# Kernel optimization log

Measured on AMD Instinct MI355X. Metric: run time of the kernel, lower is better.

Reference implementation:

```python
import jax, jax.numpy as jnp
import numpy as np

B, LQ, LK, C = 16, 1024, 1024, 512
WH = int(LQ ** 0.5)  # 32


def setup_inputs() -> dict:
    key = jax.random.key(0)
    ks = jax.random.split(key, 6)
    s1 = 1.0 / np.sqrt(LK)
    return {
        "query": jax.random.normal(ks[0], (B, LQ, C), jnp.float32),
        "key": jax.random.normal(ks[1], (B, LK, C), jnp.float32),
        "value": jax.random.normal(ks[2], (B, LK, C), jnp.float32),
        # nn.Linear weights, stored [out_features, in_features] like torch
        "w1": jax.random.normal(ks[3], (LK, LK), jnp.float32) * s1,
        "w2": jax.random.normal(ks[4], (LK, LK), jnp.float32) * s1,
        "w3": jax.random.normal(ks[5], (1, LK), jnp.float32) * s1,
    }


def reference(query, key, value, w1, w2, w3):
    # cosine-similarity matrix (computed under no_grad in the original)
    q = query / 100.0
    k = key / 100.0
    qn = jnp.sqrt(jnp.sum(q * q, axis=-1))[:, :, None]   # [B, LQ, 1]
    kn = jnp.sqrt(jnp.sum(k * k, axis=-1))[:, None, :]   # [B, 1, LK]
    outer = qn * kn                                       # rank-1 outer product [B, LQ, LK]
    upper = jnp.einsum('bqc,bkc->bqk', q, k)              # [B, LQ, LK]
    similar_rev = jax.lax.stop_gradient(upper / (outer + 1e-6))

    # 3-layer MLP gating over the LK axis -> scalar weight per query row
    h = jax.nn.gelu(jnp.einsum('bqk,ok->bqo', similar_rev, w1), approximate=False)
    h = jax.nn.gelu(jnp.einsum('bqk,ok->bqo', h, w2), approximate=False)
    w = jnp.einsum('bqk,ok->bqo', h, w3)[..., 0]          # [B, LQ]

    # weight^T @ similar_rev / wh, then tanh -> per-key scalar gate [B, LK, 1]
    weight = jnp.einsum('bq,bqk->bk', w, similar_rev) / WH
    weight = jnp.tanh(weight)[:, :, None]

    # value modulation + residual
    return value * weight + value
```

## Files before the change

### kernel.cpp

```cpp
#include <hip/hip_runtime.h>
#include <hip/hip_bf16.h>

#define B_  16
#define LQ_ 1024
#define LK_ 1024
#define C_  512

typedef __attribute__((ext_vector_type(4))) float f32x4;
typedef __attribute__((ext_vector_type(8))) short bf16x8;

__device__ __forceinline__ float bf2f(ushort u) {
  union { unsigned int i; float f; } v; v.i = ((unsigned int)u) << 16; return v.f;
}
__device__ __forceinline__ ushort f2bf(float f) {
  union { float f; unsigned int i; } v; v.f = f;
  unsigned int r = v.i + 0x7fffu + ((v.i >> 16) & 1u);
  return (ushort)(r >> 16);
}
__device__ __forceinline__ float gelu_exact(float x) {
  return 0.5f * x * (1.0f + erff(x * 0.70710678118654752f));
}

__device__ __forceinline__ void gload_lds16(const ushort* g, ushort* l) {
  __builtin_amdgcn_global_load_lds(
      (const __attribute__((address_space(1))) void*)g,
      (__attribute__((address_space(3))) void*)l, 16, 0, 0);
}

__global__ __launch_bounds__(256) void prep_qk(const float* __restrict__ x,
                                               ushort* __restrict__ xb,
                                               float* __restrict__ norms) {
  int wid = blockIdx.x * 4 + (threadIdx.x >> 6);
  int lane = threadIdx.x & 63;
  const float* xr = x + (long)wid * C_;
  ushort* xo = xb + (long)wid * C_;
  float ss = 0.f;
#pragma unroll
  for (int i0 = 0; i0 < 2; ++i0) {
    int i = lane * 4 + i0 * 256;
    float4 v = *(const float4*)(xr + i);
    ss += v.x * v.x + v.y * v.y + v.z * v.z + v.w * v.w;
    ushort4 o;
    o.x = f2bf(v.x); o.y = f2bf(v.y); o.z = f2bf(v.z); o.w = f2bf(v.w);
    *(ushort4*)(xo + i) = o;
  }
#pragma unroll
  for (int off = 32; off > 0; off >>= 1) ss += __shfl_xor(ss, off);
  if (lane == 0) norms[wid] = sqrtf(ss);
}

__global__ __launch_bounds__(256) void conv_bf16(const float* __restrict__ x,
                                                 ushort* __restrict__ o, int n4) {
  int i = blockIdx.x * 256 + threadIdx.x;
  if (i < n4) {
    float4 v = *(const float4*)(x + (long)i * 4);
    ushort4 u;
    u.x = f2bf(v.x); u.y = f2bf(v.y); u.z = f2bf(v.z); u.w = f2bf(v.w);
    *(ushort4*)(o + (long)i * 4) = u;
  }
}

#define BK 32

template <int EPI>
__global__ __launch_bounds__(256, 2) void gemm_nt(
    const ushort* __restrict__ A, const ushort* __restrict__ Bm,
    ushort* __restrict__ Cc, int K, long sA, long sB, long sC,
    const float* __restrict__ qn, const float* __restrict__ kn) {
  int per = (int)(gridDim.x >> 3);
  int orig = blockIdx.x;
  int id = (orig & 7) * per + (orig >> 3);
  int b = id >> 6;
  int rtile = id & 63;
  const int bm = (rtile >> 3) * 128, bn = (rtile & 7) * 128;

  A += (long)b * sA;
  Bm += (long)b * sB;
  Cc += (long)b * sC;

  __shared__ ushort At[2][128][32];
  __shared__ ushort Bt[2][128][32];

  int tid = threadIdx.x;
  int lane = tid & 63, w = tid >> 6;
  int wr = w >> 1, wc = w & 1;
  int l16 = lane & 15, lhi = lane >> 4;

  f32x4 acc[4][4] = {};

  int c0 = tid, c1 = tid + 256;
  int r0 = c0 >> 2, cb0 = (c0 & 3) ^ ((r0 >> 1) & 3);
  int r1 = c1 >> 2, cb1 = (c1 & 3) ^ ((r1 >> 1) & 3);
  int wbase0 = (tid & ~63);
  int wbase1 = wbase0 + 256;

  const ushort* Ar0 = A + (long)(bm + r0) * K + cb0 * 8;
  const ushort* Ar1 = A + (long)(bm + r1) * K + cb1 * 8;
  const ushort* Br0 = Bm + (long)(bn + r0) * K + cb0 * 8;
  const ushort* Br1 = Bm + (long)(bn + r1) * K + cb1 * 8;

  const int nt = K / BK;
  {
    ushort* Ad = &At[0][0][0];
    ushort* Bd = &Bt[0][0][0];
    gload_lds16(Ar0, Ad + (size_t)wbase0 * 8);
    gload_lds16(Ar1, Ad + (size_t)wbase1 * 8);
    gload_lds16(Br0, Bd + (size_t)wbase0 * 8);
    gload_lds16(Br1, Bd + (size_t)wbase1 * 8);
  }
  __syncthreads();

  int cur = 0;
  for (int t = 0; t < nt; ++t) {
    if (t + 1 < nt) {
      int k1 = (t + 1) * BK;
      ushort* Ad = &At[cur ^ 1][0][0];
      ushort* Bd = &Bt[cur ^ 1][0][0];
      gload_lds16(Ar0 + k1, Ad + (size_t)wbase0 * 8);
      gload_lds16(Ar1 + k1, Ad + (size_t)wbase1 * 8);
      gload_lds16(Br0 + k1, Bd + (size_t)wbase0 * 8);
      gload_lds16(Br1 + k1, Bd + (size_t)wbase1 * 8);
    }

    bf16x8 af[4], bfr[4];
#pragma unroll
    for (int m = 0; m < 4; ++m) {
      int r = wr * 64 + m * 16 + l16;
      af[m] = *(const bf16x8*)&At[cur][r][(lhi ^ ((r >> 1) & 3)) * 8];
    }
#pragma unroll
    for (int n = 0; n < 4; ++n) {
      int r = wc * 64 + n * 16 + l16;
      bfr[n] = *(const bf16x8*)&Bt[cur][r][(lhi ^ ((r >> 1) & 3)) * 8];
    }
#pragma unroll
    for (int m = 0; m < 4; ++m)
#pragma unroll
      for (int n = 0; n < 4; ++n)
        acc[m][n] = __builtin_amdgcn_mfma_f32_16x16x32_bf16(af[m], bfr[n],
                                                            acc[m][n], 0, 0, 0);
    __syncthreads();
    cur ^= 1;
  }

#pragma unroll
  for (int m = 0; m < 4; ++m) {
    int row0 = bm + wr * 64 + m * 16 + lhi * 4;
#pragma unroll
    for (int n = 0; n < 4; ++n) {
      int col = bn + wc * 64 + n * 16 + l16;
#pragma unroll
      for (int r = 0; r < 4; ++r) {
        float v = acc[m][n][r];
        int grow = row0 + r;
        if (EPI == 0) {
          v = v / (qn[grow] * kn[col] + 1e-2f);
        } else {
          v = gelu_exact(v);
        }
        Cc[(long)grow * 1024 + col] = f2bf(v);
      }
    }
  }
}

__global__ __launch_bounds__(256) void wdot(const ushort* __restrict__ h2,
                                            const float* __restrict__ w3,
                                            float* __restrict__ wv) {
  int row = blockIdx.x * 4 + (threadIdx.x >> 6);
  int lane = threadIdx.x & 63;
  const ushort* hr = h2 + (long)row * LK_;
  float acc = 0.f;
#pragma unroll
  for (int i = 0; i < 2; ++i) {
    int idx = (lane + 64 * i) * 8;
    bf16x8 v = *(const bf16x8*)(hr + idx);
#pragma unroll
    for (int j = 0; j < 8; ++j) acc += bf2f((ushort)v[j]) * w3[idx + j];
  }
#pragma unroll
  for (int off = 32; off > 0; off >>= 1) acc += __shfl_xor(acc, off);
  if (lane == 0) wv[row] = acc;
}

__global__ __launch_bounds__(256) void gate_partial(const ushort* __restrict__ S,
                                                    const float* __restrict__ wv,
                                                    float* __restrict__ wraw) {
  int b = blockIdx.z;
  int k = blockIdx.x * 256 + threadIdx.x;
  int q0 = blockIdx.y * 128;
  const ushort* Sb = S + (long)b * LQ_ * LK_;
  const float* wb = wv + b * LQ_;
  float acc = 0.f;
#pragma unroll 4
  for (int q = q0; q < q0 + 128; ++q) acc += wb[q] * bf2f(Sb[(long)q * LK_ + k]);
  atomicAdd(&wraw[b * LK_ + k], acc);
}

__global__ __launch_bounds__(256) void finalize(const float* __restrict__ value,
                                                const float* __restrict__ wraw,
                                                float* __restrict__ out) {
  long i = (long)blockIdx.x * 256 + threadIdx.x;
  long e = i * 4;
  int row = (int)(e >> 9);
  float g = 1.f + tanhf(wraw[row] * (1.f / 32.f));
  float4 v = ((const float4*)value)[i];
  v.x *= g; v.y *= g; v.z *= g; v.w *= g;
  ((float4*)out)[i] = v;
}

extern "C" void kernel_launch(void* const* d_in, const int* in_sizes, int n_in,
                              void* d_out, int out_size, void* d_ws,
                              size_t ws_size, hipStream_t stream) {
  const float* query = (const float*)d_in[0];
  const float* key   = (const float*)d_in[1];
  const float* value = (const float*)d_in[2];
  const float* w1    = (const float*)d_in[3];
  const float* w2    = (const float*)d_in[4];
  const float* w3    = (const float*)d_in[5];
  float* out = (float*)d_out;

  const size_t QB_BYTES = (size_t)B_ * LQ_ * C_ * 2;
  const size_t S_BYTES  = (size_t)B_ * LQ_ * LK_ * 2;
  const size_t W_BYTES  = (size_t)LK_ * LK_ * 2;
  const size_t OFF_QB = 0;
  const size_t OFF_KB = OFF_QB + QB_BYTES;
  const size_t OFF_H2 = 0;
  const size_t OFF_S  = OFF_KB + QB_BYTES;
  const size_t OFF_H1 = OFF_S + S_BYTES;
  const size_t OFF_W1 = OFF_H1 + S_BYTES;
  const size_t OFF_W2 = OFF_W1 + W_BYTES;
  const size_t OFF_QN = OFF_W2 + W_BYTES;
  const size_t OFF_KN = OFF_QN + (size_t)B_ * LQ_ * 4;
  const size_t OFF_WV = OFF_KN + (size_t)B_ * LK_ * 4;
  const size_t OFF_WR = OFF_WV + (size_t)B_ * LQ_ * 4;
  const size_t TOTAL  = OFF_WR + (size_t)B_ * LK_ * 4;
  if (ws_size < TOTAL) return;

  char* ws = (char*)d_ws;
  ushort* Qb  = (ushort*)(ws + OFF_QB);
  ushort* Kb  = (ushort*)(ws + OFF_KB);
  ushort* S   = (ushort*)(ws + OFF_S);
  ushort* h1  = (ushort*)(ws + OFF_H1);
  ushort* h2  = (ushort*)(ws + OFF_H2);
  ushort* W1b = (ushort*)(ws + OFF_W1);
  ushort* W2b = (ushort*)(ws + OFF_W2);
  float* qn   = (float*)(ws + OFF_QN);
  float* kn   = (float*)(ws + OFF_KN);
  float* wv   = (float*)(ws + OFF_WV);
  float* wraw = (float*)(ws + OFF_WR);

  prep_qk<<<dim3(B_ * LQ_ / 4), 256, 0, stream>>>(query, Qb, qn);
  prep_qk<<<dim3(B_ * LK_ / 4), 256, 0, stream>>>(key, Kb, kn);
  conv_bf16<<<dim3(LK_ * LK_ / 4 / 256), 256, 0, stream>>>(w1, W1b, LK_ * LK_ / 4);
  conv_bf16<<<dim3(LK_ * LK_ / 4 / 256), 256, 0, stream>>>(w2, W2b, LK_ * LK_ / 4);
  hipMemsetAsync(wraw, 0, (size_t)B_ * LK_ * 4, stream);

  gemm_nt<0><<<dim3(1024), 256, 0, stream>>>(
      Qb, Kb, S, C_, (long)LQ_ * C_, (long)LK_ * C_, (long)LQ_ * LK_, qn, kn);

  gemm_nt<1><<<dim3(1024), 256, 0, stream>>>(
      S, W1b, h1, LK_, (long)LQ_ * LK_, 0L, (long)LQ_ * LK_, nullptr, nullptr);

  gemm_nt<1><<<dim3(1024), 256, 0, stream>>>(
      h1, W2b, h2, LK_, (long)LQ_ * LK_, 0L, (long)LQ_ * LK_, nullptr, nullptr);

  wdot<<<dim3(B_ * LQ_ / 4), 256, 0, stream>>>(h2, w3, wv);

  gate_partial<<<dim3(LK_ / 256, LQ_ / 128, B_), 256, 0, stream>>>(S, wv, wraw);

  finalize<<<dim3((size_t)B_ * LK_ * C_ / 4 / 256), 256, 0, stream>>>(value, wraw, out);
}
```

Baseline: 177.6 us.

## Fuse w3 dot into second MLP GEMM and coalesce GEMM output via LDS

The second MLP GEMM now applies GELU and reduces against w3 in its epilogue, accumulating the per-row weight with atomics. This removes the h2 intermediate's global write and re-read and the separate wdot kernel. The other GEMMs stage bf16 output tiles through swizzled shared memory so global stores are coalesced 16-byte vectors, and launch bounds now target four blocks per CU. The norm indexing also gains a per-batch offset. The atomics add a memset and make the result order-nondeterministic, and the tighter register budget risks spills.

```diff
diff --git a/kernel.cpp b/kernel.cpp
--- a/kernel.cpp
+++ b/kernel.cpp
@@ -63,10 +63,11 @@
 #define BK 32
 
 template <int EPI>
-__global__ __launch_bounds__(256, 2) void gemm_nt(
+__device__ __forceinline__ void gemm128_body(
     const ushort* __restrict__ A, const ushort* __restrict__ Bm,
     ushort* __restrict__ Cc, int K, long sA, long sB, long sC,
-    const float* __restrict__ qn, const float* __restrict__ kn) {
+    const float* __restrict__ qn, const float* __restrict__ kn,
+    const float* __restrict__ w3v, float* __restrict__ wv) {
   int per = (int)(gridDim.x >> 3);
   int orig = blockIdx.x;
   int id = (orig & 7) * per + (orig >> 3);
@@ -76,10 +77,8 @@
 
   A += (long)b * sA;
   Bm += (long)b * sB;
-  Cc += (long)b * sC;
-
-  __shared__ ushort At[2][128][32];
-  __shared__ ushort Bt[2][128][32];
+
+  __shared__ ushort smem[16384];
 
   int tid = threadIdx.x;
   int lane = tid & 63, w = tid >> 6;
@@ -91,8 +90,8 @@
   int c0 = tid, c1 = tid + 256;
   int r0 = c0 >> 2, cb0 = (c0 & 3) ^ ((r0 >> 1) & 3);
   int r1 = c1 >> 2, cb1 = (c1 & 3) ^ ((r1 >> 1) & 3);
-  int wbase0 = (tid & ~63);
-  int wbase1 = wbase0 + 256;
+  int wb0 = (tid & ~63) * 8;
+  int wb1 = wb0 + 256 * 8;
 
   const ushort* Ar0 = A + (long)(bm + r0) * K + cb0 * 8;
   const ushort* Ar1 = A + (long)(bm + r1) * K + cb1 * 8;
@@ -100,38 +99,35 @@
   const ushort* Br1 = Bm + (long)(bn + r1) * K + cb1 * 8;
 
   const int nt = K / BK;
-  {
-    ushort* Ad = &At[0][0][0];
-    ushort* Bd = &Bt[0][0][0];
-    gload_lds16(Ar0, Ad + (size_t)wbase0 * 8);
-    gload_lds16(Ar1, Ad + (size_t)wbase1 * 8);
-    gload_lds16(Br0, Bd + (size_t)wbase0 * 8);
-    gload_lds16(Br1, Bd + (size_t)wbase1 * 8);
-  }
+  gload_lds16(Ar0, smem + wb0);
+  gload_lds16(Ar1, smem + wb1);
+  gload_lds16(Br0, smem + 8192 + wb0);
+  gload_lds16(Br1, smem + 8192 + wb1);
   __syncthreads();
 
   int cur = 0;
   for (int t = 0; t < nt; ++t) {
     if (t + 1 < nt) {
       int k1 = (t + 1) * BK;
-      ushort* Ad = &At[cur ^ 1][0][0];
-      ushort* Bd = &Bt[cur ^ 1][0][0];
-      gload_lds16(Ar0 + k1, Ad + (size_t)wbase0 * 8);
-      gload_lds16(Ar1 + k1, Ad + (size_t)wbase1 * 8);
-      gload_lds16(Br0 + k1, Bd + (size_t)wbase0 * 8);
-      gload_lds16(Br1 + k1, Bd + (size_t)wbase1 * 8);
-    }
-
+      int nx = (cur ^ 1) * 4096;
+      gload_lds16(Ar0 + k1, smem + nx + wb0);
+      gload_lds16(Ar1 + k1, smem + nx + wb1);
+      gload_lds16(Br0 + k1, smem + 8192 + nx + wb0);
+      gload_lds16(Br1 + k1, smem + 8192 + nx + wb1);
+    }
+
+    const ushort* Ac = smem + cur * 4096;
+    const ushort* Bc = smem + 8192 + cur * 4096;
     bf16x8 af[4], bfr[4];
 #pragma unroll
     for (int m = 0; m < 4; ++m) {
       int r = wr * 64 + m * 16 + l16;
-      af[m] = *(const bf16x8*)&At[cur][r][(lhi ^ ((r >> 1) & 3)) * 8];
+      af[m] = *(const bf16x8*)(Ac + r * 32 + ((lhi ^ ((r >> 1) & 3)) * 8));
     }
 #pragma unroll
     for (int n = 0; n < 4; ++n) {
       int r = wc * 64 + n * 16 + l16;
-      bfr[n] = *(const bf16x8*)&Bt[cur][r][(lhi ^ ((r >> 1) & 3)) * 8];
+      bfr[n] = *(const bf16x8*)(Bc + r * 32 + ((lhi ^ ((r >> 1) & 3)) * 8));
     }
 #pragma unroll
     for (int m = 0; m < 4; ++m)
@@ -143,44 +139,81 @@
     cur ^= 1;
   }
 
-#pragma unroll
-  for (int m = 0; m < 4; ++m) {
-    int row0 = bm + wr * 64 + m * 16 + lhi * 4;
-#pragma unroll
-    for (int n = 0; n < 4; ++n) {
-      int col = bn + wc * 64 + n * 16 + l16;
-#pragma unroll
-      for (int r = 0; r < 4; ++r) {
-        float v = acc[m][n][r];
-        int grow = row0 + r;
-        if (EPI == 0) {
-          v = v / (qn[grow] * kn[col] + 1e-2f);
-        } else {
-          v = gelu_exact(v);
+  if constexpr (EPI == 2) {
+    float* wvb = wv + (long)b * LQ_;
+    float w3c[4];
+#pragma unroll
+    for (int n = 0; n < 4; ++n) w3c[n] = w3v[bn + wc * 64 + n * 16 + l16];
+#pragma unroll
+    for (int m = 0; m < 4; ++m)
+#pragma unroll
+      for (int rr = 0; rr < 4; ++rr) {
+        float s = 0.f;
+#pragma unroll
+        for (int n = 0; n < 4; ++n)
+          s += gelu_exact(acc[m][n][rr]) * w3c[n];
+        s += __shfl_xor(s, 1);
+        s += __shfl_xor(s, 2);
+        s += __shfl_xor(s, 4);
+        s += __shfl_xor(s, 8);
+        if (l16 == 0)
+          atomicAdd(&wvb[bm + wr * 64 + m * 16 + lhi * 4 + rr], s);
+      }
+  } else {
+    Cc += (long)b * sC;
+    const float* qnb = qn + (long)b * LQ_;
+    const float* knb = kn + (long)b * LK_;
+#pragma unroll
+    for (int m = 0; m < 4; ++m) {
+#pragma unroll
+      for (int rr = 0; rr < 4; ++rr) {
+        int lrow = wr * 64 + m * 16 + lhi * 4 + rr;
+#pragma unroll
+        for (int n = 0; n < 4; ++n) {
+          int col = wc * 64 + n * 16 + l16;
+          float v = acc[m][n][rr];
+          if (EPI == 0) {
+            v = v / (qnb[bm + lrow] * knb[bn + col] + 1e-2f);
+          } else {
+            v = gelu_exact(v);
+          }
+          int pc = (col >> 3) ^ (lrow & 15);
+          smem[lrow * 128 + pc * 8 + (col & 7)] = f2bf(v);
         }
-        Cc[(long)grow * 1024 + col] = f2bf(v);
       }
     }
+    __syncthreads();
+#pragma unroll
+    for (int p = 0; p < 8; ++p) {
+      int row = p * 16 + (tid >> 4);
+      int cj = tid & 15;
+      int pc = cj ^ (row & 15);
+      bf16x8 v = *(const bf16x8*)(smem + row * 128 + pc * 8);
+      *(bf16x8*)&Cc[(long)(bm + row) * 1024 + bn + cj * 8] = v;
+    }
   }
 }
 
-__global__ __launch_bounds__(256) void wdot(const ushort* __restrict__ h2,
-                                            const float* __restrict__ w3,
-                                            float* __restrict__ wv) {
-  int row = blockIdx.x * 4 + (threadIdx.x >> 6);
-  int lane = threadIdx.x & 63;
-  const ushort* hr = h2 + (long)row * LK_;
-  float acc = 0.f;
-#pragma unroll
-  for (int i = 0; i < 2; ++i) {
-    int idx = (lane + 64 * i) * 8;
-    bf16x8 v = *(const bf16x8*)(hr + idx);
-#pragma unroll
-    for (int j = 0; j < 8; ++j) acc += bf2f((ushort)v[j]) * w3[idx + j];
-  }
-#pragma unroll
-  for (int off = 32; off > 0; off >>= 1) acc += __shfl_xor(acc, off);
-  if (lane == 0) wv[row] = acc;
+__global__ __launch_bounds__(256, 4) void gemm_s(
+    const ushort* __restrict__ A, const ushort* __restrict__ Bm,
+    ushort* __restrict__ Cc, const float* __restrict__ qn,
+    const float* __restrict__ kn) {
+  gemm128_body<0>(A, Bm, Cc, C_, (long)LQ_ * C_, (long)LK_ * C_,
+                  (long)LQ_ * LK_, qn, kn, nullptr, nullptr);
+}
+
+__global__ __launch_bounds__(256, 4) void gemm_h1(
+    const ushort* __restrict__ A, const ushort* __restrict__ Bm,
+    ushort* __restrict__ Cc) {
+  gemm128_body<1>(A, Bm, Cc, LK_, (long)LQ_ * LK_, 0L, (long)LQ_ * LK_,
+                  nullptr, nullptr, nullptr, nullptr);
+}
+
+__global__ __launch_bounds__(256, 4) void gemm_h2w(
+    const ushort* __restrict__ A, const ushort* __restrict__ Bm,
+    const float* __restrict__ w3v, float* __restrict__ wv) {
+  gemm128_body<2>(A, Bm, nullptr, LK_, (long)LQ_ * LK_, 0L, 0L,
+                  nullptr, nullptr, w3v, wv);
 }
 
 __global__ __launch_bounds__(256) void gate_partial(const ushort* __restrict__ S,
@@ -225,7 +258,6 @@
   const size_t W_BYTES  = (size_t)LK_ * LK_ * 2;
   const size_t OFF_QB = 0;
   const size_t OFF_KB = OFF_QB + QB_BYTES;
-  const size_t OFF_H2 = 0;
   const size_t OFF_S  = OFF_KB + QB_BYTES;
   const size_t OFF_H1 = OFF_S + S_BYTES;
   const size_t OFF_W1 = OFF_H1 + S_BYTES;
@@ -242,7 +274,6 @@
   ushort* Kb  = (ushort*)(ws + OFF_KB);
   ushort* S   = (ushort*)(ws + OFF_S);
   ushort* h1  = (ushort*)(ws + OFF_H1);
-  ushort* h2  = (ushort*)(ws + OFF_H2);
   ushort* W1b = (ushort*)(ws + OFF_W1);
   ushort* W2b = (ushort*)(ws + OFF_W2);
   float* qn   = (float*)(ws + OFF_QN);
@@ -255,17 +286,13 @@
   conv_bf16<<<dim3(LK_ * LK_ / 4 / 256), 256, 0, stream>>>(w1, W1b, LK_ * LK_ / 4);
   conv_bf16<<<dim3(LK_ * LK_ / 4 / 256), 256, 0, stream>>>(w2, W2b, LK_ * LK_ / 4);
   hipMemsetAsync(wraw, 0, (size_t)B_ * LK_ * 4, stream);
-
-  gemm_nt<0><<<dim3(1024), 256, 0, stream>>>(
-      Qb, Kb, S, C_, (long)LQ_ * C_, (long)LK_ * C_, (long)LQ_ * LK_, qn, kn);
-
-  gemm_nt<1><<<dim3(1024), 256, 0, stream>>>(
-      S, W1b, h1, LK_, (long)LQ_ * LK_, 0L, (long)LQ_ * LK_, nullptr, nullptr);
-
-  gemm_nt<1><<<dim3(1024), 256, 0, stream>>>(
-      h1, W2b, h2, LK_, (long)LQ_ * LK_, 0L, (long)LQ_ * LK_, nullptr, nullptr);
-
-  wdot<<<dim3(B_ * LQ_ / 4), 256, 0, stream>>>(h2, w3, wv);
+  hipMemsetAsync(wv, 0, (size_t)B_ * LQ_ * 4, stream);
+
+  gemm_s<<<dim3(1024), 256, 0, stream>>>(Qb, Kb, S, qn, kn);
+
+  gemm_h1<<<dim3(1024), 256, 0, stream>>>(S, W1b, h1);
+
+  gemm_h2w<<<dim3(1024), 256, 0, stream>>>(h1, W2b, w3, wv);
 
   gate_partial<<<dim3(LK_ / 256, LQ_ / 128, B_), 256, 0, stream>>>(S, wv, wraw);
 
```

Measured after the change: 183.8 us. 3.5% more time.
